# Kernel tuning notes

Measured on AMD Instinct MI355X. Metric: run time of the kernel, lower is better.

The kernel has to match this reference:

```python
import jax, jax.numpy as jnp
import numpy as np

N = 20000   # nodes
E = 240000  # edges (avg degree 12)
D = 128     # hidden_dim
H = 4       # heads
C = D // H  # head dim = 32
L = 3       # layers


def _ln(x, g, b):
    m = x.mean(-1, keepdims=True)
    v = ((x - m) ** 2).mean(-1, keepdims=True)
    return (x - m) / jnp.sqrt(v + 1e-5) * g + b


def setup_inputs() -> dict:
    key = jax.random.key(0)
    ks = iter(jax.random.split(key, 64))
    def w(shape, s=0.02):
        return jax.random.normal(next(ks), shape, jnp.float32) * s
    z = lambda shape: jnp.zeros(shape, jnp.float32)
    o = lambda shape: jnp.ones(shape, jnp.float32)
    inp = {
        'xyz': jax.random.normal(next(ks), (N, 3), jnp.float32) * 10.0,
        'attr': jax.random.uniform(next(ks), (N, 1), jnp.float32),
        'edge_index': jax.random.randint(next(ks), (2, E), 0, N, jnp.int32),
        # input encoder
        'enc_W': w((4, D)), 'enc_b': z((D,)), 'enc_g': o((D,)), 'enc_bb': z((D,)),
        # relative position MLP
        'pos_W1': w((3, D)), 'pos_b1': z((D,)), 'pos_g': o((D,)), 'pos_bb': z((D,)),
        'pos_W2': w((D, D)), 'pos_b2': z((D,)),
        # TransformerConv per-layer params (stacked over L)
        'Wq': w((L, D, D)), 'bq': z((L, D)),
        'Wk': w((L, D, D)), 'bk': z((L, D)),
        'Wv': w((L, D, D)), 'bv': z((L, D)),
        'We': w((L, D, D)),                 # lin_edge (no bias in PyG)
        'Wskip': w((L, D, D)), 'bskip': z((L, D)),
        'Wbeta': w((L, 3 * D, 1)),          # lin_beta (no bias)
        'ln1_g': o((L, D)), 'ln1_b': z((L, D)),
        'ln2_g': o((L, D)), 'ln2_b': z((L, D)),
        'fW1': w((L, D, 2 * D)), 'fb1': z((L, 2 * D)),
        'fW2': w((L, 2 * D, D)), 'fb2': z((L, D)),
        # heads
        'cls_W1': w((D, D // 2)), 'cls_b1': z((D // 2,)),
        'cls_W2': w((D // 2, 4)), 'cls_b2': z((4,)),
        'box_W1': w((D, D // 2)), 'box_b1': z((D // 2,)),
        'box_W2': w((D // 2, 7)), 'box_b2': z((7,)),
    }
    return inp


def reference(xyz, attr, edge_index, enc_W, enc_b, enc_g, enc_bb,
              pos_W1, pos_b1, pos_g, pos_bb, pos_W2, pos_b2,
              Wq, bq, Wk, bk, Wv, bv, We, Wskip, bskip, Wbeta,
              ln1_g, ln1_b, ln2_g, ln2_b, fW1, fb1, fW2, fb2,
              cls_W1, cls_b1, cls_W2, cls_b2, box_W1, box_b1, box_W2, box_b2):
    n = xyz.shape[0]
    src, dst = edge_index[0], edge_index[1]  # x_j = x[src], x_i = x[dst]; aggregate at dst
    inv_sqrt_c = 1.0 / float(np.sqrt(C))

    # input encoder: Linear -> LayerNorm -> ReLU
    x = jnp.concatenate([xyz, attr], axis=-1)
    x = jax.nn.relu(_ln(x @ enc_W + enc_b, enc_g, enc_bb))

    # relative position encoding per edge: i, j = edge_index; rel = xyz[j] - xyz[i]
    rel = xyz[dst] - xyz[src]
    e = jax.nn.relu(_ln(rel @ pos_W1 + pos_b1, pos_g, pos_bb)) @ pos_W2 + pos_b2  # [E, D]

    for l in range(L):
        # TransformerConv (beta=True, concat=True, edge_dim=D), eval mode (no dropout)
        q = (x @ Wq[l] + bq[l]).reshape(n, H, C)
        k = (x @ Wk[l] + bk[l]).reshape(n, H, C)
        v = (x @ Wv[l] + bv[l]).reshape(n, H, C)
        ee = (e @ We[l]).reshape(-1, H, C)          # [E, H, C]
        kj = k[src] + ee                             # edge-conditioned keys
        alpha = (q[dst] * kj).sum(-1) * inv_sqrt_c   # [E, H]
        amax = jax.ops.segment_max(alpha, dst, num_segments=n)
        ex = jnp.exp(alpha - amax[dst])
        den = jax.ops.segment_sum(ex, dst, num_segments=n)
        a = ex / den[dst]                            # scatter softmax over in-edges of dst
        msg = (v[src] + ee) * a[:, :, None]
        out = jax.ops.segment_sum(msg, dst, num_segments=n).reshape(n, D)
        # beta-gated skip
        r = x @ Wskip[l] + bskip[l]
        beta = jax.nn.sigmoid(jnp.concatenate([out, r, out - r], axis=-1) @ Wbeta[l])  # [N,1]
        out = beta * r + (1.0 - beta) * out
        # residual + LN + FFN + residual + LN
        x = _ln(out + x, ln1_g[l], ln1_b[l])
        h = jax.nn.gelu(x @ fW1[l] + fb1[l], approximate=False) @ fW2[l] + fb2[l]
        x = _ln(h + x, ln2_g[l], ln2_b[l])

    cls_logits = jax.nn.relu(x @ cls_W1 + cls_b1) @ cls_W2 + cls_b2  # [N, 4]
    box_pred = jax.nn.relu(x @ box_W1 + box_b1) @ box_W2 + box_b2    # [N, 7]
    return (cls_logits, box_pred)
```

## Files before the change

kernel.cpp:

```cpp
#include <hip/hip_runtime.h>
#include <hip/hip_bf16.h>
#include <math.h>

#define DD 128

typedef __attribute__((ext_vector_type(8))) short short8;
typedef __attribute__((ext_vector_type(4))) float f32x4;


__device__ __forceinline__ unsigned short f2b(float f) {
    unsigned u = __float_as_uint(f);
    return (unsigned short)((u + 0x7FFFu + ((u >> 16) & 1u)) >> 16);
}
__device__ __forceinline__ float b2f(unsigned short b) {
    return __uint_as_float(((unsigned)b) << 16);
}
__device__ __forceinline__ unsigned packbf(float a, float b) {
    return (unsigned)f2b(a) | ((unsigned)f2b(b) << 16);
}

__device__ __forceinline__ void redsum2_128(float& a, float& b) {
    #pragma unroll
    for (int off = 32; off > 0; off >>= 1) {
        a += __shfl_down(a, off);
        b += __shfl_down(b, off);
    }
    __shared__ float sa[2], sb[2];
    int w = threadIdx.x >> 6;
    if ((threadIdx.x & 63) == 0) { sa[w] = a; sb[w] = b; }
    __syncthreads();
    a = sa[0] + sa[1];
    b = sb[0] + sb[1];
    __syncthreads();
}


__global__ void packw12_kernel(const float* __restrict__ Wq, const float* __restrict__ Wk,
                               const float* __restrict__ Wv, const float* __restrict__ Ws,
                               unsigned* __restrict__ Wp) {
    int bid = blockIdx.x, y = blockIdx.y, d = threadIdx.x;
    int l = y >> 2, wt = y & 3;
    const float* W = (wt == 0 ? Wq : wt == 1 ? Wk : wt == 2 ? Wv : Ws) + (size_t)l * DD * DD;
    float w0 = W[(size_t)(2 * bid) * DD + d];
    float w1 = W[(size_t)(2 * bid + 1) * DD + d];
    Wp[y * 8192 + (((d << 6) + bid) ^ ((d & 7) << 2))] = packbf(w0, w1);
}

__global__ void wcombp_kernel(const float* __restrict__ W2, const float* __restrict__ b2,
                              const float* __restrict__ We, unsigned* __restrict__ Wp,
                              float* __restrict__ b2We) {
    int bid = blockIdx.x, y = blockIdx.y, d = threadIdx.x;
    const float* We_l = We + (size_t)y * DD * DD;
    __shared__ float sa0[DD], sa1[DD];
    if (bid < 64) { sa0[d] = W2[(2 * bid) * DD + d]; sa1[d] = W2[(2 * bid + 1) * DD + d]; }
    else          { sa0[d] = b2[d]; sa1[d] = 0.f; }
    __syncthreads();
    float acc0 = 0.f, acc1 = 0.f;
    #pragma unroll 8
    for (int kk = 0; kk < DD; ++kk) {
        float w = We_l[kk * DD + d];
        acc0 += sa0[kk] * w;
        acc1 += sa1[kk] * w;
    }
    if (bid < 64) Wp[y * 8192 + (((d << 6) + bid) ^ ((d & 7) << 2))] = packbf(acc0, acc1);
    else          b2We[y * DD + d] = acc0;
}

struct B4 { const float* b[4]; };

__global__ __launch_bounds__(256) void proj_kernel(
        const unsigned short* __restrict__ xb, const unsigned* __restrict__ Wp4, B4 bias,
        unsigned short* __restrict__ qkv, float* __restrict__ rbuf, int rowsN, int rtN,
        const float4* __restrict__ rel4, const float* __restrict__ pw,
        const float* __restrict__ bbp, const unsigned* __restrict__ Wpee,
        const float* __restrict__ biasee, unsigned short* __restrict__ eeout,
        int rowsE, int rtE) {
    __shared__ unsigned Bt[8192];
    __shared__ float sc[640];
    const int t = threadIdx.x;
    const int lane = t & 63, wid = t >> 6;
    const int kqo = (lane >> 4) * 8;

    if ((int)blockIdx.x < rtE) {
        const int rowBase = (int)blockIdx.x << 6;
        #pragma unroll
        for (int i = 0; i < 8; ++i)
            *(uint4*)&Bt[(i * 256 + t) * 4] = *(const uint4*)&Wpee[(i * 256 + t) * 4];
        for (int i = t; i < 640; i += 256)
            sc[i] = (i < 512) ? pw[i] : bbp[i - 512];
        int arow = rowBase + wid * 16 + (lane & 15);
        if (arow > rowsE - 1) arow = rowsE - 1;
        float4 rv = rel4[arow];
        __syncthreads();
        short8 a[4];
        #pragma unroll
        for (int kc = 0; kc < 4; ++kc) {
            union { short8 s; unsigned short u[8]; } cv;
            #pragma unroll
            for (int j = 0; j < 8; ++j) {
                int d = kc * 32 + kqo + j;
                float y = fmaf(rv.x, sc[d], fmaf(rv.y, sc[128 + d], fmaf(rv.z, sc[256 + d], sc[384 + d])));
                cv.u[j] = f2b(fmaxf(fmaf(y, rv.w, sc[512 + d]), 0.f));
            }
            a[kc] = cv.s;
        }
        f32x4 acc[8];
        #pragma unroll
        for (int i = 0; i < 8; ++i) acc[i] = (f32x4){0.f, 0.f, 0.f, 0.f};
        #pragma unroll
        for (int ng = 0; ng < 8; ++ng) {
            int col = ng * 16 + (lane & 15);
            #pragma unroll
            for (int kc = 0; kc < 4; ++kc) {
                int kidx = kc * 16 + (lane >> 4) * 4;
                const short8 b = *(const short8*)((const char*)Bt +
                        ((((col << 6) + kidx) ^ ((col & 7) << 2)) << 2));
                acc[ng] = __builtin_amdgcn_mfma_f32_16x16x32_bf16(a[kc], b, acc[ng], 0, 0, 0);
            }
        }
        __syncthreads();
        unsigned short* sb16 = (unsigned short*)Bt;
        #pragma unroll
        for (int ng = 0; ng < 8; ++ng) {
            int col = ng * 16 + (lane & 15);
            float bv = biasee[col];
            int cp = col >> 1, cb = col & 1;
            #pragma unroll
            for (int r = 0; r < 4; ++r) {
                int row = wid * 16 + (lane >> 4) * 4 + r;
                sb16[((row << 6) + (cp ^ ((row & 7) << 2))) * 2 + cb] = f2b(acc[ng][r] + bv);
            }
        }
        __syncthreads();
        unsigned* outw = (unsigned*)eeout;
        #pragma unroll
        for (int i = 0; i < 4; ++i) {
            int j = i * 1024 + t * 4;
            int row = j >> 6, cp = j & 63;
            uint4 v = *(const uint4*)&Bt[(row << 6) + (cp ^ ((row & 7) << 2))];
            int grow = rowBase + row;
            if (grow < rowsE) *(uint4*)&outw[(size_t)grow * 64 + cp] = v;
        }
    } else {
        int bidx = (int)blockIdx.x - rtE;
        const int y = bidx / rtN;
        const int rowBase = (bidx % rtN) << 6;
        const unsigned* Wp = Wp4 + y * 8192;
        #pragma unroll
        for (int i = 0; i < 8; ++i)
            *(uint4*)&Bt[(i * 256 + t) * 4] = *(const uint4*)&Wp[(i * 256 + t) * 4];
        int arow = rowBase + wid * 16 + (lane & 15);
        if (arow > rowsN - 1) arow = rowsN - 1;
        short8 a[4];
        #pragma unroll
        for (int kc = 0; kc < 4; ++kc)
            a[kc] = *(const short8*)(xb + (size_t)arow * DD + kc * 32 + kqo);
        __syncthreads();
        f32x4 acc[8];
        #pragma unroll
        for (int i = 0; i < 8; ++i) acc[i] = (f32x4){0.f, 0.f, 0.f, 0.f};
        #pragma unroll
        for (int ng = 0; ng < 8; ++ng) {
            int col = ng * 16 + (lane & 15);
            #pragma unroll
            for (int kc = 0; kc < 4; ++kc) {
                int kidx = kc * 16 + (lane >> 4) * 4;
                const short8 b = *(const short8*)((const char*)Bt +
                        ((((col << 6) + kidx) ^ ((col & 7) << 2)) << 2));
                acc[ng] = __builtin_amdgcn_mfma_f32_16x16x32_bf16(a[kc], b, acc[ng], 0, 0, 0);
            }
        }
        const float* bs = bias.b[y];
        if (y == 3) {
            #pragma unroll
            for (int ng = 0; ng < 8; ++ng) {
                int col = ng * 16 + (lane & 15);
                float bv = bs[col];
                #pragma unroll
                for (int r = 0; r < 4; ++r) {
                    int grow = rowBase + wid * 16 + (lane >> 4) * 4 + r;
                    if (grow < rowsN) rbuf[(size_t)grow * DD + col] = acc[ng][r] + bv;
                }
            }
            return;
        }
        __syncthreads();
        unsigned short* sb16 = (unsigned short*)Bt;
        #pragma unroll
        for (int ng = 0; ng < 8; ++ng) {
            int col = ng * 16 + (lane & 15);
            float bv = bs[col];
            int cp = col >> 1, cb = col & 1;
            #pragma unroll
            for (int r = 0; r < 4; ++r) {
                int row = wid * 16 + (lane >> 4) * 4 + r;
                sb16[((row << 6) + (cp ^ ((row & 7) << 2))) * 2 + cb] = f2b(acc[ng][r] + bv);
            }
        }
        __syncthreads();
        unsigned* outw = (unsigned*)qkv;
        #pragma unroll
        for (int i = 0; i < 4; ++i) {
            int j = i * 1024 + t * 4;
            int row = j >> 6, cp = j & 63;
            uint4 v = *(const uint4*)&Bt[(row << 6) + (cp ^ ((row & 7) << 2))];
            int grow = rowBase + row;
            if (grow < rowsN) *(uint4*)&outw[(size_t)grow * 192 + (y << 6) + cp] = v;
        }
    }
}

template <int ACT>
__global__ __launch_bounds__(256) void mgemm(
        const unsigned short* __restrict__ A, const float* __restrict__ W,
        const float* __restrict__ bias, unsigned short* __restrict__ out,
        int rows, int K, int Dout) {
    __shared__ unsigned Bt[8192];
    const int t = threadIdx.x;
    const int rowBase = blockIdx.x << 6;
    const int colBase = blockIdx.y << 7;
    const int lane = t & 63, wid = t >> 6;
    f32x4 acc[8];
    #pragma unroll
    for (int i = 0; i < 8; ++i) acc[i] = (f32x4){0.f, 0.f, 0.f, 0.f};
    int arow = rowBase + wid * 16 + (lane & 15);
    if (arow > rows - 1) arow = rows - 1;
    const int kqo = (lane >> 4) * 8;
    for (int k0 = 0; k0 < K; k0 += 128) {
        if (k0) __syncthreads();
        #pragma unroll 8
        for (int it = 0; it < 32; ++it) {
            int idx = it * 256 + t;
            int n = idx & 127, kp = idx >> 7;
            int krow = k0 + kp * 2;
            float w0 = W[(size_t)krow * Dout + colBase + n];
            float w1 = W[(size_t)(krow + 1) * Dout + colBase + n];
            Bt[((n << 6) + kp) ^ ((n & 7) << 2)] = packbf(w0, w1);
        }
        __syncthreads();
        short8 a[4];
        #pragma unroll
        for (int kc = 0; kc < 4; ++kc)
            a[kc] = *(const short8*)(A + (size_t)arow * K + k0 + kc * 32 + kqo);
        #pragma unroll
        for (int ng = 0; ng < 8; ++ng) {
            int col = ng * 16 + (lane & 15);
            #pragma unroll
            for (int kc = 0; kc < 4; ++kc) {
                int kidx = kc * 16 + (lane >> 4) * 4;
                const short8 b = *(const short8*)((const char*)Bt +
                        ((((col << 6) + kidx) ^ ((col & 7) << 2)) << 2));
                acc[ng] = __builtin_amdgcn_mfma_f32_16x16x32_bf16(a[kc], b, acc[ng], 0, 0, 0);
            }
        }
    }
    __syncthreads();
    unsigned short* sb16 = (unsigned short*)Bt;
    #pragma unroll
    for (int ng = 0; ng < 8; ++ng) {
        int col = ng * 16 + (lane & 15);
        float bv = bias[colBase + col];
        int cp = col >> 1, cb = col & 1;
        #pragma unroll
        for (int r = 0; r < 4; ++r) {
            int row = wid * 16 + (lane >> 4) * 4 + r;
            float val = acc[ng][r] + bv;
            if (ACT == 1) val = 0.5f * val * (1.f + erff(val * 0.70710678118654752f));
            else if (ACT == 2) val = fmaxf(val, 0.f);
            sb16[((row << 6) + (cp ^ ((row & 7) << 2))) * 2 + cb] = f2b(val);
        }
    }
    __syncthreads();
    unsigned* outw = (unsigned*)out;
    const int strideU = Dout >> 1, cbU = colBase >> 1;
    #pragma unroll
    for (int i = 0; i < 4; ++i) {
        int j = i * 1024 + t * 4;
        int row = j >> 6, cp = j & 63;
        uint4 v = *(const uint4*)&Bt[(row << 6) + (cp ^ ((row & 7) << 2))];
        int grow = rowBase + row;
        if (grow < rows) *(uint4*)&outw[(size_t)grow * strideU + cbU + cp] = v;
    }
}

__global__ __launch_bounds__(256) void mgemm_ln(
        const unsigned short* __restrict__ h1, const float* __restrict__ W,
        const float* __restrict__ bias, const float* __restrict__ g,
        const float* __restrict__ bb, float* __restrict__ x,
        unsigned short* __restrict__ xb, int rows) {
    __shared__ unsigned Bt[8192];
    const int t = threadIdx.x;
    const int rowBase = blockIdx.x << 6;
    const int lane = t & 63, wid = t >> 6;
    f32x4 acc[8];
    #pragma unroll
    for (int i = 0; i < 8; ++i) acc[i] = (f32x4){0.f, 0.f, 0.f, 0.f};
    int arow = rowBase + wid * 16 + (lane & 15);
    if (arow > rows - 1) arow = rows - 1;
    const int kqo = (lane >> 4) * 8;
    for (int k0 = 0; k0 < 256; k0 += 128) {
        if (k0) __syncthreads();
        #pragma unroll 8
        for (int it = 0; it < 32; ++it) {
            int idx = it * 256 + t;
            int n = idx & 127, kp = idx >> 7;
            int krow = k0 + kp * 2;
            float w0 = W[(size_t)krow * DD + n];
            float w1 = W[(size_t)(krow + 1) * DD + n];
            Bt[((n << 6) + kp) ^ ((n & 7) << 2)] = packbf(w0, w1);
        }
        __syncthreads();
        short8 a[4];
        #pragma unroll
        for (int kc = 0; kc < 4; ++kc)
            a[kc] = *(const short8*)(h1 + (size_t)arow * 256 + k0 + kc * 32 + kqo);
        #pragma unroll
        for (int ng = 0; ng < 8; ++ng) {
            int col = ng * 16 + (lane & 15);
            #pragma unroll
            for (int kc = 0; kc < 4; ++kc) {
                int kidx = kc * 16 + (lane >> 4) * 4;
                const short8 b = *(const short8*)((const char*)Bt +
                        ((((col << 6) + kidx) ^ ((col & 7) << 2)) << 2));
                acc[ng] = __builtin_amdgcn_mfma_f32_16x16x32_bf16(a[kc], b, acc[ng], 0, 0, 0);
            }
        }
    }
    float tt[8][4];
    float rs[4] = {0.f, 0.f, 0.f, 0.f}, rs2[4] = {0.f, 0.f, 0.f, 0.f};
    #pragma unroll
    for (int ng = 0; ng < 8; ++ng) {
        int col = ng * 16 + (lane & 15);
        float bv = bias[col];
        #pragma unroll
        for (int r = 0; r < 4; ++r) {
            int grow = rowBase + wid * 16 + (lane >> 4) * 4 + r;
            float xo = (grow < rows) ? x[(size_t)grow * DD + col] : 0.f;
            float v = acc[ng][r] + bv + xo;
            tt[ng][r] = v;
            rs[r] += v;
            rs2[r] += v * v;
        }
    }
    #pragma unroll
    for (int r = 0; r < 4; ++r) {
        #pragma unroll
        for (int m = 1; m < 16; m <<= 1) {
            rs[r] += __shfl_xor(rs[r], m);
            rs2[r] += __shfl_xor(rs2[r], m);
        }
    }
    __syncthreads();
    unsigned short* sb16 = (unsigned short*)Bt;
    #pragma unroll
    for (int ng = 0; ng < 8; ++ng) {
        int col = ng * 16 + (lane & 15);
        float gg = g[col], bbb = bb[col];
        int cp = col >> 1, cb = col & 1;
        #pragma unroll
        for (int r = 0; r < 4; ++r) {
            int grow = rowBase + wid * 16 + (lane >> 4) * 4 + r;
            float mean = rs[r] * (1.f / DD);
            float var = rs2[r] * (1.f / DD) - mean * mean;
            float val = (tt[ng][r] - mean) * rsqrtf(var + 1e-5f) * gg + bbb;
            if (grow < rows) x[(size_t)grow * DD + col] = val;
            int row = wid * 16 + (lane >> 4) * 4 + r;
            sb16[((row << 6) + (cp ^ ((row & 7) << 2))) * 2 + cb] = f2b(val);
        }
    }
    __syncthreads();
    unsigned* outw = (unsigned*)xb;
    #pragma unroll
    for (int i = 0; i < 4; ++i) {
        int j = i * 1024 + t * 4;
        int row = j >> 6, cp = j & 63;
        uint4 v = *(const uint4*)&Bt[(row << 6) + (cp ^ ((row & 7) << 2))];
        int grow = rowBase + row;
        if (grow < rows) *(uint4*)&outw[(size_t)grow * 64 + cp] = v;
    }
}


__global__ void enc_kernel(const float* __restrict__ xyz, const float* __restrict__ attr,
                           const float* __restrict__ W, const float* __restrict__ b,
                           const float* __restrict__ g, const float* __restrict__ bb,
                           float* __restrict__ x, unsigned short* __restrict__ xb) {
    int i = blockIdx.x, d = threadIdx.x;
    __shared__ float sin4[4];
    if (d < 3) sin4[d] = xyz[i * 3 + d];
    if (d == 3) sin4[3] = attr[i];
    __syncthreads();
    float y = b[d];
    #pragma unroll
    for (int kk = 0; kk < 4; ++kk) y += sin4[kk] * W[kk * DD + d];
    float s = y, s2 = y * y;
    redsum2_128(s, s2);
    float mean = s * (1.0f / DD);
    float var = s2 * (1.0f / DD) - mean * mean;
    float xn = fmaxf((y - mean) * rsqrtf(var + 1e-5f) * g[d] + bb[d], 0.f);
    x[i * DD + d] = xn;
    xb[(size_t)i * DD + d] = f2b(xn);
}

__global__ void posprep_kernel(const float* __restrict__ W1, const float* __restrict__ b1,
                               const float* __restrict__ g, float* __restrict__ pw) {
    int d = threadIdx.x;
    float w0 = W1[d], w1 = W1[DD + d], w2 = W1[2 * DD + d], b = b1[d];
    float s0 = w0, s1 = w1;
    redsum2_128(s0, s1);
    float s2 = w2, s3 = b;
    redsum2_128(s2, s3);
    float c0 = w0 - s0 * (1.f / DD), c1 = w1 - s1 * (1.f / DD);
    float c2 = w2 - s2 * (1.f / DD), bc = b - s3 * (1.f / DD);
    float gd = g[d];
    pw[d] = c0 * gd; pw[DD + d] = c1 * gd; pw[2 * DD + d] = c2 * gd; pw[3 * DD + d] = bc * gd;
    float p0 = c0 * c0, p1 = c0 * c1; redsum2_128(p0, p1);
    float p2 = c0 * c2, p3 = c1 * c1; redsum2_128(p2, p3);
    float p4 = c1 * c2, p5 = c2 * c2; redsum2_128(p4, p5);
    float p6 = c0 * bc, p7 = c1 * bc; redsum2_128(p6, p7);
    float p8 = c2 * bc, p9 = bc * bc; redsum2_128(p8, p9);
    if (d == 0) {
        pw[512] = p0 * (1.f / DD); pw[513] = p1 * (1.f / DD); pw[514] = p2 * (1.f / DD);
        pw[515] = p3 * (1.f / DD); pw[516] = p4 * (1.f / DD); pw[517] = p5 * (1.f / DD);
        pw[518] = p6 * (1.f / DD); pw[519] = p7 * (1.f / DD); pw[520] = p8 * (1.f / DD);
        pw[521] = p9 * (1.f / DD);
    }
}


__global__ void hist_kernel(const int* __restrict__ ei, int* __restrict__ deg, int E) {
    int e = blockIdx.x * blockDim.x + threadIdx.x;
    if (e < E) atomicAdd(&deg[ei[E + e]], 1);
}

__global__ void scan_kernel(const int* __restrict__ deg, int* __restrict__ ptr, int n) {
    __shared__ int partial[1024];
    int t = threadIdx.x;
    int CH = (n + 1023) >> 10;
    int beg = t * CH;
    int end = beg + CH; if (end > n) end = n;
    int s = 0;
    for (int i = beg; i < end; ++i) s += deg[i];
    partial[t] = s;
    __syncthreads();
    for (int off = 1; off < 1024; off <<= 1) {
        int add = (t >= off) ? partial[t - off] : 0;
        __syncthreads();
        partial[t] += add;
        __syncthreads();
    }
    int base = (t == 0) ? 0 : partial[t - 1];
    for (int i = beg; i < end; ++i) {
        ptr[i] = base;
        base += deg[i];
    }
    if (end == n && beg < n) ptr[n] = base;
}

__global__ void scatter_kernel(const int* __restrict__ ei, const float* __restrict__ xyz,
                               const float* __restrict__ pw, const int* __restrict__ ptr,
                               int* __restrict__ cur, int* __restrict__ cs_src,
                               float4* __restrict__ rel4, int E) {
    int e = blockIdx.x * blockDim.x + threadIdx.x;
    if (e >= E) return;
    int srcn = ei[e], dstn = ei[E + e];
    int p = atomicAdd(&cur[dstn], 1);
    int slot = ptr[dstn] + p;
    cs_src[slot] = srcn;
    float r0 = xyz[dstn * 3]     - xyz[srcn * 3];
    float r1 = xyz[dstn * 3 + 1] - xyz[srcn * 3 + 1];
    float r2 = xyz[dstn * 3 + 2] - xyz[srcn * 3 + 2];
    float var = pw[512] * r0 * r0 + pw[515] * r1 * r1 + pw[517] * r2 * r2
              + 2.f * (pw[513] * r0 * r1 + pw[514] * r0 * r2 + pw[516] * r1 * r2)
              + 2.f * (pw[518] * r0 + pw[519] * r1 + pw[520] * r2) + pw[521];
    rel4[slot] = make_float4(r0, r1, r2, rsqrtf(var + 1e-5f));
}

__global__ __launch_bounds__(256) void aggc_kernel(
        const unsigned* __restrict__ qkv, const unsigned* __restrict__ ee,
        const int* __restrict__ ptr, const int* __restrict__ cs_src,
        const float* __restrict__ r, const float* __restrict__ Wb,
        const float* __restrict__ g1, const float* __restrict__ b1,
        float* __restrict__ x, unsigned* __restrict__ xbw, int N) {
    int node = (blockIdx.x << 2) + (threadIdx.x >> 6);
    if (node >= N) return;
    const int lane = threadIdx.x & 63;
    unsigned qp = qkv[(size_t)node * 192 + lane];
    float q0 = b2f((unsigned short)qp), q1 = b2f((unsigned short)(qp >> 16));
    int beg = ptr[node], end = ptr[node + 1];
    float s = 0.f, a0 = 0.f, a1 = 0.f;
    unsigned epN = 0, kpN = 0, vpN = 0;
    if (beg < end) {
        int j = cs_src[beg];
        epN = __builtin_nontemporal_load(&ee[(size_t)beg * 64 + lane]);
        kpN = qkv[(size_t)j * 192 + 64 + lane];
        vpN = qkv[(size_t)j * 192 + 128 + lane];
    }
    for (int idx = beg; idx < end; ++idx) {
        unsigned ep = epN, kp = kpN, vp = vpN;
        int nidx = idx + 1;
        if (nidx < end) {
            int jn = cs_src[nidx];
            epN = __builtin_nontemporal_load(&ee[(size_t)nidx * 64 + lane]);
            kpN = qkv[(size_t)jn * 192 + 64 + lane];
            vpN = qkv[(size_t)jn * 192 + 128 + lane];
        }
        float e0 = b2f((unsigned short)ep), e1 = b2f((unsigned short)(ep >> 16));
        float kj0 = b2f((unsigned short)kp) + e0;
        float kj1 = b2f((unsigned short)(kp >> 16)) + e1;
        float p = q0 * kj0 + q1 * kj1;
        p += __shfl_xor(p, 1); p += __shfl_xor(p, 2);
        p += __shfl_xor(p, 4); p += __shfl_xor(p, 8);
        float w = __expf(p * 0.17677669529663687f);
        s += w;
        a0 += (b2f((unsigned short)vp) + e0) * w;
        a1 += (b2f((unsigned short)(vp >> 16)) + e1) * w;
    }
    float inv_s = (s > 0.f) ? 1.f / s : 0.f;
    float od0 = a0 * inv_s, od1 = a1 * inv_s;
    float2 rd = *(const float2*)&r[(size_t)node * DD + lane * 2];
    float2 wb0 = *(const float2*)&Wb[lane * 2];
    float2 wb1 = *(const float2*)&Wb[DD + lane * 2];
    float2 wb2 = *(const float2*)&Wb[2 * DD + lane * 2];
    float part = od0 * wb0.x + rd.x * wb1.x + (od0 - rd.x) * wb2.x
               + od1 * wb0.y + rd.y * wb1.y + (od1 - rd.y) * wb2.y;
    #pragma unroll
    for (int m = 1; m < 64; m <<= 1) part += __shfl_xor(part, m);
    float beta = 1.f / (1.f + __expf(-part));
    float2 xo = *(const float2*)&x[(size_t)node * DD + lane * 2];
    float t0 = beta * rd.x + (1.f - beta) * od0 + xo.x;
    float t1 = beta * rd.y + (1.f - beta) * od1 + xo.y;
    float ss = t0 + t1, ss2 = t0 * t0 + t1 * t1;
    #pragma unroll
    for (int m = 1; m < 64; m <<= 1) { ss += __shfl_xor(ss, m); ss2 += __shfl_xor(ss2, m); }
    float mean = ss * (1.f / DD);
    float var = ss2 * (1.f / DD) - mean * mean;
    float inv = rsqrtf(var + 1e-5f);
    float2 gg = *(const float2*)&g1[lane * 2];
    float2 bbv = *(const float2*)&b1[lane * 2];
    float2 res;
    res.x = (t0 - mean) * inv * gg.x + bbv.x;
    res.y = (t1 - mean) * inv * gg.y + bbv.y;
    *(float2*)&x[(size_t)node * DD + lane * 2] = res;
    xbw[(size_t)node * 64 + lane] = packbf(res.x, res.y);
}


__global__ void headprep_kernel(const float* __restrict__ cW1, const float* __restrict__ cb1,
                                const float* __restrict__ bW1, const float* __restrict__ bb1,
                                float* __restrict__ W1cat, float* __restrict__ b1cat) {
    int kk = blockIdx.x, d = threadIdx.x;
    W1cat[kk * DD + d] = (d < 64) ? cW1[kk * 64 + d] : bW1[kk * 64 + (d - 64)];
    if (kk == 0) b1cat[d] = (d < 64) ? cb1[d] : bb1[d - 64];
}

__global__ __launch_bounds__(256) void heads2_kernel(
        const unsigned* __restrict__ hh, const float* __restrict__ cW2,
        const float* __restrict__ cb2, const float* __restrict__ bW2,
        const float* __restrict__ bb2, float* __restrict__ outc,
        float* __restrict__ outb, int N) {
    int node = (blockIdx.x << 2) + (threadIdx.x >> 6);
    if (node >= N) return;
    const int lane = threadIdx.x & 63;
    unsigned hp = hh[(size_t)node * 64 + lane];
    float h0 = b2f((unsigned short)hp), h1 = b2f((unsigned short)(hp >> 16));
    bool isCls = lane < 32;
    int dd = isCls ? 2 * lane : 2 * lane - 128 + 64;
    float c[4], bx[7];
    #pragma unroll
    for (int j = 0; j < 4; ++j)
        c[j] = isCls ? h0 * cW2[dd * 4 + j] + h1 * cW2[(dd + 1) * 4 + j] : 0.f;
    #pragma unroll
    for (int j = 0; j < 7; ++j)
        bx[j] = isCls ? 0.f : h0 * bW2[dd * 7 + j] + h1 * bW2[(dd + 1) * 7 + j];
    #pragma unroll
    for (int m = 1; m < 32; m <<= 1) {
        #pragma unroll
        for (int j = 0; j < 4; ++j) c[j] += __shfl_xor(c[j], m);
        #pragma unroll
        for (int j = 0; j < 7; ++j) bx[j] += __shfl_xor(bx[j], m);
    }
    if (lane == 0) {
        #pragma unroll
        for (int j = 0; j < 4; ++j) outc[(size_t)node * 4 + j] = c[j] + cb2[j];
    } else if (lane == 32) {
        #pragma unroll
        for (int j = 0; j < 7; ++j) outb[(size_t)node * 7 + j] = bx[j] + bb2[j];
    }
}

extern "C" void kernel_launch(void* const* d_in, const int* in_sizes, int n_in,
                              void* d_out, int out_size, void* d_ws, size_t ws_size,
                              hipStream_t stream) {
    const float* xyz   = (const float*)d_in[0];
    const float* attr  = (const float*)d_in[1];
    const int*   ei    = (const int*)d_in[2];
    const float* encW  = (const float*)d_in[3];
    const float* encb  = (const float*)d_in[4];
    const float* encg  = (const float*)d_in[5];
    const float* encbb = (const float*)d_in[6];
    const float* posW1 = (const float*)d_in[7];
    const float* posb1 = (const float*)d_in[8];
    const float* posg  = (const float*)d_in[9];
    const float* posbb = (const float*)d_in[10];
    const float* posW2 = (const float*)d_in[11];
    const float* posb2 = (const float*)d_in[12];
    const float* Wq    = (const float*)d_in[13];
    const float* bq    = (const float*)d_in[14];
    const float* Wk    = (const float*)d_in[15];
    const float* bk    = (const float*)d_in[16];
    const float* Wv    = (const float*)d_in[17];
    const float* bv    = (const float*)d_in[18];
    const float* We    = (const float*)d_in[19];
    const float* Wskip = (const float*)d_in[20];
    const float* bskip = (const float*)d_in[21];
    const float* Wbeta = (const float*)d_in[22];
    const float* ln1g  = (const float*)d_in[23];
    const float* ln1b  = (const float*)d_in[24];
    const float* ln2g  = (const float*)d_in[25];
    const float* ln2b  = (const float*)d_in[26];
    const float* fW1   = (const float*)d_in[27];
    const float* fb1   = (const float*)d_in[28];
    const float* fW2   = (const float*)d_in[29];
    const float* fb2   = (const float*)d_in[30];
    const float* cW1   = (const float*)d_in[31];
    const float* cb1   = (const float*)d_in[32];
    const float* cW2   = (const float*)d_in[33];
    const float* cb2   = (const float*)d_in[34];
    const float* bW1   = (const float*)d_in[35];
    const float* bb1   = (const float*)d_in[36];
    const float* bW2   = (const float*)d_in[37];
    const float* bb2   = (const float*)d_in[38];

    const int N = in_sizes[0] / 3;
    const int E = in_sizes[2] / 2;

    size_t off = 0;
    auto alloc = [&](size_t nelem) {
        char* p = (char*)d_ws + off;
        off += nelem * sizeof(float);
        return (float*)p;
    };
    float* x     = alloc((size_t)N * DD);
    unsigned short* qkv = (unsigned short*)alloc((size_t)N * 192);
    float* r     = alloc((size_t)N * DD);
    unsigned short* h1 = (unsigned short*)alloc((size_t)N * 128);
    unsigned short* xb = (unsigned short*)alloc((size_t)N * 64);
    float4* rel4 = (float4*)alloc((size_t)E * 4);
    unsigned short* eeb = (unsigned short*)alloc((size_t)E * 64);
    unsigned* W2Wep = (unsigned*)alloc(3 * 8192);
    float* b2We  = alloc(3 * DD);
    unsigned* Wp12 = (unsigned*)alloc(12 * 8192);
    float* pw    = alloc(544);
    float* W1cat = alloc(DD * DD);
    float* b1cat = alloc(DD);
    int* deg     = (int*)alloc(N);
    int* ptr     = (int*)alloc(N + 1);
    int* cur     = (int*)alloc(N);
    int* cs_src  = (int*)alloc(E);

    const int rtN = (N + 63) / 64;
    const int rtE = (E + 63) / 64;

    enc_kernel<<<N, DD, 0, stream>>>(xyz, attr, encW, encb, encg, encbb, x, xb);
    hipMemsetAsync(deg, 0, N * sizeof(int), stream);
    hipMemsetAsync(cur, 0, N * sizeof(int), stream);
    hist_kernel<<<(E + 255) / 256, 256, 0, stream>>>(ei, deg, E);
    scan_kernel<<<1, 1024, 0, stream>>>(deg, ptr, N);
    posprep_kernel<<<1, DD, 0, stream>>>(posW1, posb1, posg, pw);
    scatter_kernel<<<(E + 255) / 256, 256, 0, stream>>>(ei, xyz, pw, ptr, cur, cs_src, rel4, E);
    wcombp_kernel<<<dim3(65, 3), DD, 0, stream>>>(posW2, posb2, We, W2Wep, b2We);
    packw12_kernel<<<dim3(64, 12), DD, 0, stream>>>(Wq, Wk, Wv, Wskip, Wp12);
    headprep_kernel<<<DD, DD, 0, stream>>>(cW1, cb1, bW1, bb1, W1cat, b1cat);

    for (int l = 0; l < 3; ++l) {
        const float* Wb_l = Wbeta + (size_t)l * 3 * DD;
        const float* fW1_l = fW1 + (size_t)l * DD * 256;
        const float* fW2_l = fW2 + (size_t)l * 256 * DD;
        B4 bs;
        bs.b[0] = bq + l * DD; bs.b[1] = bk + l * DD;
        bs.b[2] = bv + l * DD; bs.b[3] = bskip + l * DD;

        proj_kernel<<<rtE + 4 * rtN, 256, 0, stream>>>(
            xb, Wp12 + (size_t)l * 4 * 8192, bs, qkv, r, N, rtN,
            rel4, pw, posbb, W2Wep + l * 8192, b2We + l * DD, eeb, E, rtE);

        aggc_kernel<<<(N + 3) / 4, 256, 0, stream>>>((const unsigned*)qkv, (const unsigned*)eeb,
                                                     ptr, cs_src, r, Wb_l,
                                                     ln1g + l * DD, ln1b + l * DD,
                                                     x, (unsigned*)xb, N);

        mgemm<1><<<dim3(rtN, 2), 256, 0, stream>>>(xb, fW1_l, fb1 + l * 256, h1, N, DD, 256);
        mgemm_ln<<<rtN, 256, 0, stream>>>(h1, fW2_l, fb2 + l * DD,
                                          ln2g + l * DD, ln2b + l * DD, x, xb, N);
    }

    float* outc  = (float*)d_out;
    float* outbx = (float*)d_out + (size_t)N * 4;
    mgemm<2><<<dim3(rtN, 1), 256, 0, stream>>>(xb, W1cat, b1cat, h1, N, DD, DD);
    heads2_kernel<<<(N + 3) / 4, 256, 0, stream>>>((const unsigned*)h1, cW2, cb2, bW2, bb2,
                                                   outc, outbx, N);
}
```

Before: 455.1 us.

## Fuse FFN GEMMs into one kernel and split edge aggregation across two waves

The two FFN matmuls (GELU up-projection and down-projection plus residual LayerNorm) are merged into one kernel. The GELU intermediate now stays in shared memory instead of making a global round trip through h1. Separately, the attention aggregation kernel now assigns two waves per node, each taking alternate edges, and combines their partial sums through shared memory to raise memory-level parallelism. The trade-offs are doubled shared memory per block in the FFN kernel, which lowers occupancy, and half the lanes idling through the epilogue of the aggregation kernel.

```diff
diff --git a/kernel.cpp b/kernel.cpp
--- a/kernel.cpp
+++ b/kernel.cpp
@@ -283,37 +283,41 @@
     }
 }
 
-__global__ __launch_bounds__(256) void mgemm_ln(
-        const unsigned short* __restrict__ h1, const float* __restrict__ W,
-        const float* __restrict__ bias, const float* __restrict__ g,
-        const float* __restrict__ bb, float* __restrict__ x,
+__global__ __launch_bounds__(256) void ffn_fused(
+        const unsigned short* __restrict__ xbin, const float* __restrict__ W1,
+        const float* __restrict__ b1f, const float* __restrict__ W2,
+        const float* __restrict__ b2f, const float* __restrict__ g,
+        const float* __restrict__ bbn, float* __restrict__ x,
         unsigned short* __restrict__ xb, int rows) {
     __shared__ unsigned Bt[8192];
+    __shared__ unsigned h1t[8192];
     const int t = threadIdx.x;
     const int rowBase = blockIdx.x << 6;
     const int lane = t & 63, wid = t >> 6;
-    f32x4 acc[8];
-    #pragma unroll
-    for (int i = 0; i < 8; ++i) acc[i] = (f32x4){0.f, 0.f, 0.f, 0.f};
+    const int kqo = (lane >> 4) * 8;
     int arow = rowBase + wid * 16 + (lane & 15);
     if (arow > rows - 1) arow = rows - 1;
-    const int kqo = (lane >> 4) * 8;
-    for (int k0 = 0; k0 < 256; k0 += 128) {
-        if (k0) __syncthreads();
+
+    short8 a[4];
+    #pragma unroll
+    for (int kc = 0; kc < 4; ++kc)
+        a[kc] = *(const short8*)(xbin + (size_t)arow * DD + kc * 32 + kqo);
+
+    unsigned short* h16 = (unsigned short*)h1t;
+    for (int half = 0; half < 2; ++half) {
+        if (half) __syncthreads();
         #pragma unroll 8
         for (int it = 0; it < 32; ++it) {
             int idx = it * 256 + t;
             int n = idx & 127, kp = idx >> 7;
-            int krow = k0 + kp * 2;
-            float w0 = W[(size_t)krow * DD + n];
-            float w1 = W[(size_t)(krow + 1) * DD + n];
+            float w0 = W1[(size_t)(2 * kp) * 256 + half * 128 + n];
+            float w1 = W1[(size_t)(2 * kp + 1) * 256 + half * 128 + n];
             Bt[((n << 6) + kp) ^ ((n & 7) << 2)] = packbf(w0, w1);
         }
         __syncthreads();
-        short8 a[4];
-        #pragma unroll
-        for (int kc = 0; kc < 4; ++kc)
-            a[kc] = *(const short8*)(h1 + (size_t)arow * 256 + k0 + kc * 32 + kqo);
+        f32x4 acc[8];
+        #pragma unroll
+        for (int i = 0; i < 8; ++i) acc[i] = (f32x4){0.f, 0.f, 0.f, 0.f};
         #pragma unroll
         for (int ng = 0; ng < 8; ++ng) {
             int col = ng * 16 + (lane & 15);
@@ -325,18 +329,65 @@
                 acc[ng] = __builtin_amdgcn_mfma_f32_16x16x32_bf16(a[kc], b, acc[ng], 0, 0, 0);
             }
         }
+        #pragma unroll
+        for (int ng = 0; ng < 8; ++ng) {
+            int col = half * 128 + ng * 16 + (lane & 15);
+            float bv = b1f[col];
+            int cp = col >> 1, cb = col & 1;
+            #pragma unroll
+            for (int r = 0; r < 4; ++r) {
+                int row = wid * 16 + (lane >> 4) * 4 + r;
+                float val = acc[ng][r] + bv;
+                val = 0.5f * val * (1.f + erff(val * 0.70710678118654752f));
+                h16[((row << 7) + (cp ^ ((row & 7) << 2))) * 2 + cb] = f2b(val);
+            }
+        }
+    }
+    f32x4 accF[8];
+    #pragma unroll
+    for (int i = 0; i < 8; ++i) accF[i] = (f32x4){0.f, 0.f, 0.f, 0.f};
+    const int lrow = wid * 16 + (lane & 15);
+    for (int c = 0; c < 2; ++c) {
+        __syncthreads();
+        #pragma unroll 8
+        for (int it = 0; it < 32; ++it) {
+            int idx = it * 256 + t;
+            int n = idx & 127, kp = idx >> 7;
+            int krow = c * 128 + kp * 2;
+            float w0 = W2[(size_t)krow * DD + n];
+            float w1 = W2[(size_t)(krow + 1) * DD + n];
+            Bt[((n << 6) + kp) ^ ((n & 7) << 2)] = packbf(w0, w1);
+        }
+        __syncthreads();
+        short8 ah[4];
+        #pragma unroll
+        for (int kc = 0; kc < 4; ++kc) {
+            int cp4 = c * 64 + kc * 16 + (lane >> 4) * 4;
+            ah[kc] = *(const short8*)&h1t[(lrow << 7) + (cp4 ^ ((lrow & 7) << 2))];
+        }
+        #pragma unroll
+        for (int ng = 0; ng < 8; ++ng) {
+            int col = ng * 16 + (lane & 15);
+            #pragma unroll
+            for (int kc = 0; kc < 4; ++kc) {
+                int kidx = kc * 16 + (lane >> 4) * 4;
+                const short8 b = *(const short8*)((const char*)Bt +
+                        ((((col << 6) + kidx) ^ ((col & 7) << 2)) << 2));
+                accF[ng] = __builtin_amdgcn_mfma_f32_16x16x32_bf16(ah[kc], b, accF[ng], 0, 0, 0);
+            }
+        }
     }
     float tt[8][4];
     float rs[4] = {0.f, 0.f, 0.f, 0.f}, rs2[4] = {0.f, 0.f, 0.f, 0.f};
     #pragma unroll
     for (int ng = 0; ng < 8; ++ng) {
         int col = ng * 16 + (lane & 15);
-        float bv = bias[col];
+        float bv = b2f[col];
         #pragma unroll
         for (int r = 0; r < 4; ++r) {
             int grow = rowBase + wid * 16 + (lane >> 4) * 4 + r;
             float xo = (grow < rows) ? x[(size_t)grow * DD + col] : 0.f;
-            float v = acc[ng][r] + bv + xo;
+            float v = accF[ng][r] + bv + xo;
             tt[ng][r] = v;
             rs[r] += v;
             rs2[r] += v * v;
@@ -355,7 +406,7 @@
     #pragma unroll
     for (int ng = 0; ng < 8; ++ng) {
         int col = ng * 16 + (lane & 15);
-        float gg = g[col], bbb = bb[col];
+        float gg = g[col], bbb = bbn[col];
         int cp = col >> 1, cb = col & 1;
         #pragma unroll
         for (int r = 0; r < 4; ++r) {
@@ -482,23 +533,35 @@
         const float* __restrict__ r, const float* __restrict__ Wb,
         const float* __restrict__ g1, const float* __restrict__ b1,
         float* __restrict__ x, unsigned* __restrict__ xbw, int N) {
-    int node = (blockIdx.x << 2) + (threadIdx.x >> 6);
-    if (node >= N) return;
+    const int wave = threadIdx.x >> 6;
     const int lane = threadIdx.x & 63;
-    unsigned qp = qkv[(size_t)node * 192 + lane];
-    float q0 = b2f((unsigned short)qp), q1 = b2f((unsigned short)(qp >> 16));
-    int beg = ptr[node], end = ptr[node + 1];
+    const int node = ((int)blockIdx.x << 1) + (wave >> 1);
+    const int half = wave & 1;
+    __shared__ float sS[4];
+    __shared__ float sA0[4][64];
+    __shared__ float sA1[4][64];
+
     float s = 0.f, a0 = 0.f, a1 = 0.f;
+    float q0 = 0.f, q1 = 0.f;
+    int beg = 0, end = 0;
+    if (node < N) {
+        unsigned qp = qkv[(size_t)node * 192 + lane];
+        q0 = b2f((unsigned short)qp);
+        q1 = b2f((unsigned short)(qp >> 16));
+        beg = ptr[node];
+        end = ptr[node + 1];
+    }
+    int idx = beg + half;
     unsigned epN = 0, kpN = 0, vpN = 0;
-    if (beg < end) {
-        int j = cs_src[beg];
-        epN = __builtin_nontemporal_load(&ee[(size_t)beg * 64 + lane]);
+    if (idx < end) {
+        int j = cs_src[idx];
+        epN = __builtin_nontemporal_load(&ee[(size_t)idx * 64 + lane]);
         kpN = qkv[(size_t)j * 192 + 64 + lane];
         vpN = qkv[(size_t)j * 192 + 128 + lane];
     }
-    for (int idx = beg; idx < end; ++idx) {
+    for (; idx < end; idx += 2) {
         unsigned ep = epN, kp = kpN, vp = vpN;
-        int nidx = idx + 1;
+        int nidx = idx + 2;
         if (nidx < end) {
             int jn = cs_src[nidx];
             epN = __builtin_nontemporal_load(&ee[(size_t)nidx * 64 + lane]);
@@ -516,6 +579,15 @@
         a0 += (b2f((unsigned short)vp) + e0) * w;
         a1 += (b2f((unsigned short)(vp >> 16)) + e1) * w;
     }
+    sS[wave] = s;
+    sA0[wave][lane] = a0;
+    sA1[wave][lane] = a1;
+    __syncthreads();
+    if (half != 0 || node >= N) return;
+    s  = sS[wave] + sS[wave + 1];
+    a0 = sA0[wave][lane] + sA0[wave + 1][lane];
+    a1 = sA1[wave][lane] + sA1[wave + 1][lane];
+
     float inv_s = (s > 0.f) ? 1.f / s : 0.f;
     float od0 = a0 * inv_s, od1 = a1 * inv_s;
     float2 rd = *(const float2*)&r[(size_t)node * DD + lane * 2];
@@ -685,14 +757,13 @@
             xb, Wp12 + (size_t)l * 4 * 8192, bs, qkv, r, N, rtN,
             rel4, pw, posbb, W2Wep + l * 8192, b2We + l * DD, eeb, E, rtE);
 
-        aggc_kernel<<<(N + 3) / 4, 256, 0, stream>>>((const unsigned*)qkv, (const unsigned*)eeb,
+        aggc_kernel<<<(N + 1) / 2, 256, 0, stream>>>((const unsigned*)qkv, (const unsigned*)eeb,
                                                      ptr, cs_src, r, Wb_l,
                                                      ln1g + l * DD, ln1b + l * DD,
                                                      x, (unsigned*)xb, N);
 
-        mgemm<1><<<dim3(rtN, 2), 256, 0, stream>>>(xb, fW1_l, fb1 + l * 256, h1, N, DD, 256);
-        mgemm_ln<<<rtN, 256, 0, stream>>>(h1, fW2_l, fb2 + l * DD,
-                                          ln2g + l * DD, ln2b + l * DD, x, xb, N);
+        ffn_fused<<<rtN, 256, 0, stream>>>(xb, fW1_l, fb1 + l * 256, fW2_l, fb2 + l * DD,
+                                           ln2g + l * DD, ln2b + l * DD, x, xb, N);
     }
 
     float* outc  = (float*)d_out;
```

Measured after the change: 428.7 us. 5.8% less time.
